# Optimization experiments

Measured on AMD Instinct MI355X. Metric: run time of the kernel, lower is better.

## Reference

```python
import jax, jax.numpy as jnp
import numpy as np


def setup_inputs() -> dict:
    key = jax.random.key(0)
    ks = jax.random.split(key, 5)
    B, C, T, Hh, Ww = 4, 64, 8, 32, 32
    HID = 32
    s = 0.05  # weight scale for numerically sane softmax logits
    return {
        "H": jax.random.normal(ks[0], (B, C, T, Hh, Ww), dtype=jnp.float32),
        "h": jax.random.normal(ks[1], (B, C, Hh, Ww), dtype=jnp.float32),
        "w_q": jax.random.normal(ks[2], (HID, C), dtype=jnp.float32) * s,
        "w_kv": jax.random.normal(ks[3], (HID, C), dtype=jnp.float32) * s,
        "w_o": jax.random.normal(ks[4], (C, HID), dtype=jnp.float32) * s,
    }


def reference(H, h, w_q, w_kv, w_o):
    B, C, T, Hh, Ww = H.shape
    N = Hh * Ww
    Hf = H.reshape(B, C, T, N)
    # 1x1 convs are pure channel-mixing matmuls
    H_kv = jnp.einsum('dc,bctn->bdtn', w_kv, Hf)                # [B, hid, T, N]
    h_q = jnp.einsum('dc,bchw->bdhw', w_q, h).reshape(B, -1, N)  # [B, hid, N]
    h_q = h_q.transpose(0, 2, 1)                                 # [B, N, hid]
    # per-timestep scores, vectorized over t: [B, T, N, N]
    a = jnp.einsum('bnd,bdtm->btnm', h_q, H_kv)
    # remove the diagonal of each per-timestep [N, N] block
    diag = jnp.einsum('btnn->btn', a)                            # [B, T, N]
    eye = jnp.eye(N, dtype=a.dtype)
    a = a - diag[..., :, None] * eye
    # concat over t along rows, softmax over the (T*N) row axis
    att = jax.nn.softmax(a.reshape(B, T * N, N), axis=1)         # [B, T*N, N]
    h_v = jnp.einsum('bdk,bkm->bdm', H_kv.reshape(B, -1, T * N), att)  # [B, hid, N]
    h_v = jnp.einsum('cd,bdhw->bchw', w_o, h_v.reshape(B, -1, Hh, Ww))
    return (h + h_v, att)
```

## Files before the change

### kernel.cpp

```cpp
#include <hip/hip_runtime.h>

typedef short bf16x8 __attribute__((ext_vector_type(8)));
typedef float f32x4  __attribute__((ext_vector_type(4)));
typedef unsigned short ushort_t;

#define HID 32
#define CC  64
#define TT  8
#define NN  1024
#define BB  4
#define KTOT 8192
#define NKC_P 32
#define KCHUNK_P (KTOT/NKC_P)

__device__ __forceinline__ ushort_t f2b(float x) {
    unsigned int u = __float_as_uint(x);
    return (ushort_t)((u + 0x7fffu + ((u >> 16) & 1u)) >> 16);
}
__device__ __forceinline__ float b2f(ushort_t u) {
    return __uint_as_float((unsigned int)u << 16);
}

__global__ __launch_bounds__(256) void k_pre(const float* __restrict__ H,
                                             const float* __restrict__ h,
                                             const float* __restrict__ wq,
                                             const float* __restrict__ wkv,
                                             ushort_t* __restrict__ hqHI,
                                             ushort_t* __restrict__ hqLO,
                                             ushort_t* __restrict__ hkTH0,
                                             ushort_t* __restrict__ hkTH1,
                                             ushort_t* __restrict__ hkTL0,
                                             ushort_t* __restrict__ hkTL1,
                                             ushort_t* __restrict__ hkDB) {
    int bx = blockIdx.x;
    if (bx < 256) {
        int gid = bx * 256 + threadIdx.x;
        int dg = gid >> 15;
        int rest = gid & 32767;
        int b = rest >> 13, tn = rest & 8191;
        int d0 = dg << 4;
        float acc[16];
#pragma unroll
        for (int d = 0; d < 16; d++) acc[d] = 0.f;
        const float* Hb = H + (size_t)(b * CC) * KTOT + tn;
        const float* wb = wkv + d0 * CC;
#pragma unroll 8
        for (int c = 0; c < CC; c++) {
            float v = Hb[(size_t)c * KTOT];
#pragma unroll
            for (int d = 0; d < 16; d++) acc[d] += wb[d * CC + c] * v;
        }
        ushort_t thi[16], tlo[16];
#pragma unroll
        for (int d = 0; d < 16; d++) {
            ushort_t hi = f2b(acc[d]);
            thi[d] = hi;
            tlo[d] = f2b(acc[d] - b2f(hi));
        }
        size_t po = ((size_t)b * KTOT + tn) * 16;
        bf16x8* ohi = (bf16x8*)((dg ? hkTH1 : hkTH0) + po);
        bf16x8* olo = (bf16x8*)((dg ? hkTL1 : hkTL0) + po);
#pragma unroll
        for (int v8 = 0; v8 < 2; v8++) {
            bf16x8 a, l;
#pragma unroll
            for (int j = 0; j < 8; j++) { a[j] = (short)thi[v8*8+j]; l[j] = (short)tlo[v8*8+j]; }
            ohi[v8] = a; olo[v8] = l;
        }
#pragma unroll
        for (int d = 0; d < 16; d++)
            hkDB[((size_t)(b * HID) + d0 + d) * KTOT + tn] = thi[d];
    } else {
        int gid = (bx - 256) * 256 + threadIdx.x;
        int b = gid >> 10;
        float acc[HID];
#pragma unroll
        for (int d = 0; d < HID; d++) acc[d] = 0.f;
        const float* hb = h + (size_t)(b * CC) * NN + (gid & 1023);
#pragma unroll 4
        for (int c = 0; c < CC; c++) {
            float v = hb[c * NN];
#pragma unroll
            for (int d = 0; d < HID; d++) acc[d] += wq[d * CC + c] * v;
        }
        bf16x8* ohi = (bf16x8*)(hqHI + (size_t)gid * HID);
        bf16x8* olo = (bf16x8*)(hqLO + (size_t)gid * HID);
#pragma unroll
        for (int v8 = 0; v8 < 4; v8++) {
            bf16x8 thi, tlo;
#pragma unroll
            for (int j = 0; j < 8; j++) {
                float x = acc[v8 * 8 + j];
                ushort_t hi = f2b(x);
                thi[j] = (short)hi;
                tlo[j] = (short)f2b(x - b2f(hi));
            }
            ohi[v8] = thi; olo[v8] = tlo;
        }
    }
}

__global__ __launch_bounds__(512, 8) void k_psum(const ushort_t* __restrict__ hqHI,
                                                 const ushort_t* __restrict__ hkTH0,
                                                 const ushort_t* __restrict__ hkTH1,
                                                 float* __restrict__ psum) {
    int bx = blockIdx.x;
    int b = bx >> 8, mt = (bx >> 5) & 7, kc = bx & 31;
    int wave = threadIdx.x >> 6, lane = threadIdx.x & 63;
    int g = lane >> 4, c = lane & 15;
    int m = mt * 128 + wave * 16 + c;
    int t = kc >> 2;
    int nb0 = (kc & 3) << 8;

    size_t bqo = ((size_t)b * KTOT + t * NN + m) * 16 + (g & 1) * 8;
    bf16x8 bqh = *(const bf16x8*)(((g >> 1) ? hkTH1 : hkTH0) + bqo);

    const ushort_t* qhi = hqHI + ((size_t)(b << 10)) * HID;

    float csum0 = 0.f, csum1 = 0.f;
    for (int s16 = 0; s16 < KCHUNK_P / 16; s16 += 2) {
        int nbA = nb0 + s16 * 16;
        int nbB = nbA + 16;
        bf16x8 ahA = *(const bf16x8*)(qhi + (size_t)(nbA + c) * HID + 8 * g);
        bf16x8 ahB = *(const bf16x8*)(qhi + (size_t)(nbB + c) * HID + 8 * g);
        f32x4 svA = __builtin_amdgcn_mfma_f32_16x16x32_bf16(ahA, bqh, (f32x4){0.f,0.f,0.f,0.f}, 0, 0, 0);
        f32x4 svB = __builtin_amdgcn_mfma_f32_16x16x32_bf16(ahB, bqh, (f32x4){0.f,0.f,0.f,0.f}, 0, 0, 0);
        int nrowA = nbA + 4 * g;
        int nrowB = nbB + 4 * g;
#pragma unroll
        for (int r = 0; r < 4; r++) {
            float xA = (nrowA + r == m) ? 0.f : svA[r];
            float xB = (nrowB + r == m) ? 0.f : svB[r];
            csum0 += __expf(xA);
            csum1 += __expf(xB);
        }
    }
    float csum = csum0 + csum1;
    csum += __shfl_xor(csum, 16);
    csum += __shfl_xor(csum, 32);
    if (lane < 16)
        psum[(((size_t)(b * NKC_P + kc)) << 10) + mt * 128 + wave * 16 + lane] = csum;
}

__global__ __launch_bounds__(1024) void k_main(const ushort_t* __restrict__ hqHI,
                                               const ushort_t* __restrict__ hqLO,
                                               const ushort_t* __restrict__ hkTH0,
                                               const ushort_t* __restrict__ hkTH1,
                                               const ushort_t* __restrict__ hkTL0,
                                               const ushort_t* __restrict__ hkTL1,
                                               const ushort_t* __restrict__ hkDB,
                                               const float* __restrict__ psum,
                                               const float* __restrict__ h,
                                               const float* __restrict__ wo,
                                               float* __restrict__ att,
                                               float* __restrict__ out0) {
    int bx = blockIdx.x;
    int logical = ((bx & 7) << 5) | (bx >> 3);
    int b = logical >> 6, mt = logical & 63;
    int mb = mt << 4;
    int tid = threadIdx.x;
    int wave = tid >> 6, lane = tid & 63;
    int g = lane >> 4, c = lane & 15;
    int t = wave >> 1;
    int nh = (wave & 1) << 9;

    __shared__ float hvred[16][16][32];
    __shared__ float hvL[16][33];
    __shared__ __align__(16) ushort_t PT[16][16][40];

    f32x4 gs = {0.f, 0.f, 0.f, 0.f};
#pragma unroll
    for (int j = 0; j < NKC_P; j++)
        gs += *(const f32x4*)(psum + (((size_t)(b * NKC_P + j)) << 10) + mb + 4 * g);
    f32x4 vinv;
#pragma unroll
    for (int r = 0; r < 4; r++) vinv[r] = 1.0f / gs[r];

    size_t ako = ((size_t)b * KTOT + t * NN + (mb + c)) * 16 + (g & 1) * 8;
    bf16x8 akh = *(const bf16x8*)(((g >> 1) ? hkTH1 : hkTH0) + ako);
    bf16x8 akl = *(const bf16x8*)(((g >> 1) ? hkTL1 : hkTL0) + ako);

    const ushort_t* qhi = hqHI + ((size_t)(b << 10)) * HID;
    const ushort_t* qlo = hqLO + ((size_t)(b << 10)) * HID;
    const ushort_t* vb0 = hkDB + (size_t)(b * HID + c) * KTOT;
    const ushort_t* vb1 = hkDB + (size_t)(b * HID + 16 + c) * KTOT;
    float* attb = att + (size_t)b * KTOT * NN;
    ushort_t (*pt)[40] = PT[wave];

    f32x4 acc0 = {0.f,0.f,0.f,0.f}, acc1 = {0.f,0.f,0.f,0.f};

    for (int ks = 0; ks < 16; ks++) {
        int k0 = t * NN + nh + ks * 32;
#pragma unroll
        for (int half = 0; half < 2; half++) {
            int nb = nh + ks * 32 + half * 16;
            size_t qo = (size_t)(nb + c) * HID + 8 * g;
            bf16x8 qh = *(const bf16x8*)(qhi + qo);
            bf16x8 ql = *(const bf16x8*)(qlo + qo);
            f32x4 sv = __builtin_amdgcn_mfma_f32_16x16x32_bf16(akh, ql, (f32x4){0.f,0.f,0.f,0.f}, 0, 0, 0);
            sv = __builtin_amdgcn_mfma_f32_16x16x32_bf16(akl, qh, sv, 0, 0, 0);
            sv = __builtin_amdgcn_mfma_f32_16x16x32_bf16(akh, qh, sv, 0, 0, 0);
            int n = nb + c;
            float e0 = __expf((n == mb + 4 * g + 0) ? 0.f : sv[0]) * vinv[0];
            float e1 = __expf((n == mb + 4 * g + 1) ? 0.f : sv[1]) * vinv[1];
            float e2 = __expf((n == mb + 4 * g + 2) ? 0.f : sv[2]) * vinv[2];
            float e3 = __expf((n == mb + 4 * g + 3) ? 0.f : sv[3]) * vinv[3];
            f32x4 ev; ev[0] = e0; ev[1] = e1; ev[2] = e2; ev[3] = e3;
            *(f32x4*)(attb + (size_t)(t * NN + n) * NN + mb + 4 * g) = ev;
            int kl = half * 16 + c;
            pt[4 * g + 0][kl] = f2b(e0);
            pt[4 * g + 1][kl] = f2b(e1);
            pt[4 * g + 2][kl] = f2b(e2);
            pt[4 * g + 3][kl] = f2b(e3);
        }
        bf16x8 pa = *(const bf16x8*)&pt[c][8 * g];
        bf16x8 v0 = *(const bf16x8*)(vb0 + k0 + 8 * g);
        bf16x8 v1 = *(const bf16x8*)(vb1 + k0 + 8 * g);
        acc0 = __builtin_amdgcn_mfma_f32_16x16x32_bf16(pa, v0, acc0, 0, 0, 0);
        acc1 = __builtin_amdgcn_mfma_f32_16x16x32_bf16(pa, v1, acc1, 0, 0, 0);
    }

#pragma unroll
    for (int r = 0; r < 4; r++) {
        hvred[wave][4 * g + r][c]      = acc0[r];
        hvred[wave][4 * g + r][16 + c] = acc1[r];
    }
    __syncthreads();
    if (tid < 512) {
        int m = tid >> 5, d = tid & 31;
        float s = 0.f;
#pragma unroll
        for (int w = 0; w < 16; w++) s += hvred[w][m][d];
        hvL[m][d] = s;
    }
    __syncthreads();
    {
        int cc = tid >> 4, mm = tid & 15;
        float v = h[(size_t)(b * CC + cc) * NN + mb + mm];
#pragma unroll
        for (int d = 0; d < HID; d++) v += wo[cc * HID + d] * hvL[mm][d];
        out0[(size_t)(b * CC + cc) * NN + mb + mm] = v;
    }
}

extern "C" void kernel_launch(void* const* d_in, const int* in_sizes, int n_in,
                              void* d_out, int out_size, void* d_ws, size_t ws_size,
                              hipStream_t stream) {
    const float* H   = (const float*)d_in[0];
    const float* h   = (const float*)d_in[1];
    const float* wq  = (const float*)d_in[2];
    const float* wkv = (const float*)d_in[3];
    const float* wo  = (const float*)d_in[4];

    float* out0 = (float*)d_out;
    float* att  = out0 + (size_t)BB * CC * NN;

    ushort_t* hqHI  = (ushort_t*)d_ws;
    ushort_t* hqLO  = hqHI  + 131072;
    ushort_t* hkTH0 = hqLO  + 131072;
    ushort_t* hkTH1 = hkTH0 + 524288;
    ushort_t* hkTL0 = hkTH1 + 524288;
    ushort_t* hkTL1 = hkTL0 + 524288;
    ushort_t* hkDB  = hkTL1 + 524288;
    float* psum = (float*)(hkDB + 1048576);

    k_pre <<<272,  256,  0, stream>>>(H, h, wq, wkv, hqHI, hqLO,
                                      hkTH0, hkTH1, hkTL0, hkTL1, hkDB);
    k_psum<<<1024, 512,  0, stream>>>(hqHI, hkTH0, hkTH1, psum);
    k_main<<<256,  1024, 0, stream>>>(hqHI, hqLO, hkTH0, hkTH1, hkTL0, hkTL1, hkDB,
                                      psum, h, wo, att, out0);
}
```

Baseline: 85.62 us.

## Repartition k_main blocks over 32-column tiles and key halves, add output kernel

Each k_main block now covers 32 output columns and one half of the key range (n in 0-511 or 512-1023) instead of 16 columns and the full key range. Every wave now handles one timestep and one 16-column half, so the block produces a partial h_v sum for its key half. The two partial sums are written to workspace and combined in a new k_out kernel, which also applies the w_o projection and the residual add. This changes the per-block access pattern for q and att and removes the serial epilogue from k_main, at the cost of an extra launch and a workspace round trip.

```diff
diff --git a/kernel.cpp b/kernel.cpp
--- a/kernel.cpp
+++ b/kernel.cpp
@@ -150,33 +150,33 @@
                                                const ushort_t* __restrict__ hkTL1,
                                                const ushort_t* __restrict__ hkDB,
                                                const float* __restrict__ psum,
-                                               const float* __restrict__ h,
-                                               const float* __restrict__ wo,
                                                float* __restrict__ att,
-                                               float* __restrict__ out0) {
+                                               float* __restrict__ hvp) {
     int bx = blockIdx.x;
     int logical = ((bx & 7) << 5) | (bx >> 3);
-    int b = logical >> 6, mt = logical & 63;
-    int mb = mt << 4;
+    int b = logical >> 6;
+    int r6 = logical & 63;
+    int mg = r6 >> 1, kh = r6 & 1;
+    int mb32 = mg << 5;
     int tid = threadIdx.x;
     int wave = tid >> 6, lane = tid & 63;
     int g = lane >> 4, c = lane & 15;
-    int t = wave >> 1;
-    int nh = (wave & 1) << 9;
+    int t = wave >> 1, mh = wave & 1;
+    int mbw = mb32 + (mh << 4);
+    int nh = kh << 9;
 
     __shared__ float hvred[16][16][32];
-    __shared__ float hvL[16][33];
     __shared__ __align__(16) ushort_t PT[16][16][40];
 
     f32x4 gs = {0.f, 0.f, 0.f, 0.f};
 #pragma unroll
     for (int j = 0; j < NKC_P; j++)
-        gs += *(const f32x4*)(psum + (((size_t)(b * NKC_P + j)) << 10) + mb + 4 * g);
+        gs += *(const f32x4*)(psum + (((size_t)(b * NKC_P + j)) << 10) + mbw + 4 * g);
     f32x4 vinv;
 #pragma unroll
     for (int r = 0; r < 4; r++) vinv[r] = 1.0f / gs[r];
 
-    size_t ako = ((size_t)b * KTOT + t * NN + (mb + c)) * 16 + (g & 1) * 8;
+    size_t ako = ((size_t)b * KTOT + t * NN + (mbw + c)) * 16 + (g & 1) * 8;
     bf16x8 akh = *(const bf16x8*)(((g >> 1) ? hkTH1 : hkTH0) + ako);
     bf16x8 akl = *(const bf16x8*)(((g >> 1) ? hkTL1 : hkTL0) + ako);
 
@@ -201,12 +201,12 @@
             sv = __builtin_amdgcn_mfma_f32_16x16x32_bf16(akl, qh, sv, 0, 0, 0);
             sv = __builtin_amdgcn_mfma_f32_16x16x32_bf16(akh, qh, sv, 0, 0, 0);
             int n = nb + c;
-            float e0 = __expf((n == mb + 4 * g + 0) ? 0.f : sv[0]) * vinv[0];
-            float e1 = __expf((n == mb + 4 * g + 1) ? 0.f : sv[1]) * vinv[1];
-            float e2 = __expf((n == mb + 4 * g + 2) ? 0.f : sv[2]) * vinv[2];
-            float e3 = __expf((n == mb + 4 * g + 3) ? 0.f : sv[3]) * vinv[3];
+            float e0 = __expf((n == mbw + 4 * g + 0) ? 0.f : sv[0]) * vinv[0];
+            float e1 = __expf((n == mbw + 4 * g + 1) ? 0.f : sv[1]) * vinv[1];
+            float e2 = __expf((n == mbw + 4 * g + 2) ? 0.f : sv[2]) * vinv[2];
+            float e3 = __expf((n == mbw + 4 * g + 3) ? 0.f : sv[3]) * vinv[3];
             f32x4 ev; ev[0] = e0; ev[1] = e1; ev[2] = e2; ev[3] = e3;
-            *(f32x4*)(attb + (size_t)(t * NN + n) * NN + mb + 4 * g) = ev;
+            *(f32x4*)(attb + (size_t)(t * NN + n) * NN + mbw + 4 * g) = ev;
             int kl = half * 16 + c;
             pt[4 * g + 0][kl] = f2b(e0);
             pt[4 * g + 1][kl] = f2b(e1);
@@ -226,20 +226,39 @@
         hvred[wave][4 * g + r][16 + c] = acc1[r];
     }
     __syncthreads();
-    if (tid < 512) {
-        int m = tid >> 5, d = tid & 31;
+    {
+        int m32 = tid >> 5, d = tid & 31;
+        int mhh = m32 >> 4, ml = m32 & 15;
         float s = 0.f;
 #pragma unroll
-        for (int w = 0; w < 16; w++) s += hvred[w][m][d];
-        hvL[m][d] = s;
+        for (int tt = 0; tt < 8; tt++) s += hvred[tt * 2 + mhh][ml][d];
+        hvp[(((size_t)(kh * 4 + b) << 10) + mb32 + m32) * HID + d] = s;
+    }
+}
+
+__global__ __launch_bounds__(512) void k_out(const float* __restrict__ h,
+                                             const float* __restrict__ wo,
+                                             const float* __restrict__ hvp,
+                                             float* __restrict__ out0) {
+    int bx = blockIdx.x;
+    int b = bx >> 6, mt = bx & 63;
+    int m0 = mt * 16;
+    int tid = threadIdx.x;
+    __shared__ float hvL[16][33];
+    {
+        int mm = tid >> 5, d = tid & 31;
+        size_t i0 = ((size_t)(b << 10) + m0 + mm) * HID + d;
+        hvL[mm][d] = hvp[i0] + hvp[((size_t)4 << 15) + i0];
     }
     __syncthreads();
-    {
-        int cc = tid >> 4, mm = tid & 15;
-        float v = h[(size_t)(b * CC + cc) * NN + mb + mm];
-#pragma unroll
-        for (int d = 0; d < HID; d++) v += wo[cc * HID + d] * hvL[mm][d];
-        out0[(size_t)(b * CC + cc) * NN + mb + mm] = v;
+#pragma unroll
+    for (int i0 = 0; i0 < 2; i0++) {
+        int i = i0 * 512 + tid;
+        int c = i >> 4, mm = i & 15;
+        float v = h[(size_t)(b * CC + c) * NN + m0 + mm];
+#pragma unroll
+        for (int d = 0; d < HID; d++) v += wo[c * HID + d] * hvL[mm][d];
+        out0[(size_t)(b * CC + c) * NN + m0 + mm] = v;
     }
 }
 
@@ -263,10 +282,12 @@
     ushort_t* hkTL1 = hkTL0 + 524288;
     ushort_t* hkDB  = hkTL1 + 524288;
     float* psum = (float*)(hkDB + 1048576);
+    float* hvp  = psum + 131072;
 
     k_pre <<<272,  256,  0, stream>>>(H, h, wq, wkv, hqHI, hqLO,
                                       hkTH0, hkTH1, hkTL0, hkTL1, hkDB);
     k_psum<<<1024, 512,  0, stream>>>(hqHI, hkTH0, hkTH1, psum);
     k_main<<<256,  1024, 0, stream>>>(hqHI, hqLO, hkTH0, hkTH1, hkTL0, hkTL1, hkDB,
-                                      psum, h, wo, att, out0);
-}
+                                      psum, att, hvp);
+    k_out <<<256,  512,  0, stream>>>(h, wo, hvp, out0);
+}
```

Result: no change. 86.67 us (+1.2%).

## Split main kernel into hv-accumulation blocks and separate att-writer blocks

Applied to the files above, without the earlier changes.

Replaces the single main kernel with a combined launch. The first 256 blocks compute the hv accumulation at single-pass bf16 precision (only the hi parts of q and k), and the other 2048 blocks recompute scores at 3-pass precision and write the large att tensor. A small kernel now reduces the partial softmax sums to reciprocals once, so blocks no longer each re-reduce psum. The aim is to spread the store-bound att writes across many more blocks while the hv path does less MFMA work. In exchange, QK scores are computed twice, and the lower-precision P used for hv may change accuracy.

```diff
diff --git a/kernel.cpp b/kernel.cpp
--- a/kernel.cpp
+++ b/kernel.cpp
@@ -142,104 +142,149 @@
         psum[(((size_t)(b * NKC_P + kc)) << 10) + mt * 128 + wave * 16 + lane] = csum;
 }
 
-__global__ __launch_bounds__(1024) void k_main(const ushort_t* __restrict__ hqHI,
-                                               const ushort_t* __restrict__ hqLO,
-                                               const ushort_t* __restrict__ hkTH0,
-                                               const ushort_t* __restrict__ hkTH1,
-                                               const ushort_t* __restrict__ hkTL0,
-                                               const ushort_t* __restrict__ hkTL1,
-                                               const ushort_t* __restrict__ hkDB,
-                                               const float* __restrict__ psum,
-                                               const float* __restrict__ h,
-                                               const float* __restrict__ wo,
-                                               float* __restrict__ att,
-                                               float* __restrict__ out0) {
+__global__ __launch_bounds__(256) void k_inv(const float* __restrict__ psum,
+                                             float* __restrict__ inv) {
+    int gid = blockIdx.x * 256 + threadIdx.x;
+    int b = gid >> 10, m = gid & 1023;
+    float s = 0.f;
+#pragma unroll
+    for (int kc = 0; kc < NKC_P; kc++)
+        s += psum[(((size_t)(b * NKC_P + kc)) << 10) + m];
+    inv[gid] = 1.0f / s;
+}
+
+__global__ __launch_bounds__(512) void k_mega(const ushort_t* __restrict__ hqHI,
+                                              const ushort_t* __restrict__ hqLO,
+                                              const ushort_t* __restrict__ hkTH0,
+                                              const ushort_t* __restrict__ hkTH1,
+                                              const ushort_t* __restrict__ hkTL0,
+                                              const ushort_t* __restrict__ hkTL1,
+                                              const ushort_t* __restrict__ hkDB,
+                                              const float* __restrict__ inv,
+                                              const float* __restrict__ h,
+                                              const float* __restrict__ wo,
+                                              float* __restrict__ att,
+                                              float* __restrict__ out0) {
     int bx = blockIdx.x;
-    int logical = ((bx & 7) << 5) | (bx >> 3);
-    int b = logical >> 6, mt = logical & 63;
-    int mb = mt << 4;
     int tid = threadIdx.x;
     int wave = tid >> 6, lane = tid & 63;
     int g = lane >> 4, c = lane & 15;
-    int t = wave >> 1;
-    int nh = (wave & 1) << 9;
-
-    __shared__ float hvred[16][16][32];
-    __shared__ float hvL[16][33];
-    __shared__ __align__(16) ushort_t PT[16][16][40];
-
-    f32x4 gs = {0.f, 0.f, 0.f, 0.f};
-#pragma unroll
-    for (int j = 0; j < NKC_P; j++)
-        gs += *(const f32x4*)(psum + (((size_t)(b * NKC_P + j)) << 10) + mb + 4 * g);
-    f32x4 vinv;
-#pragma unroll
-    for (int r = 0; r < 4; r++) vinv[r] = 1.0f / gs[r];
-
-    size_t ako = ((size_t)b * KTOT + t * NN + (mb + c)) * 16 + (g & 1) * 8;
-    bf16x8 akh = *(const bf16x8*)(((g >> 1) ? hkTH1 : hkTH0) + ako);
-    bf16x8 akl = *(const bf16x8*)(((g >> 1) ? hkTL1 : hkTL0) + ako);
-
-    const ushort_t* qhi = hqHI + ((size_t)(b << 10)) * HID;
-    const ushort_t* qlo = hqLO + ((size_t)(b << 10)) * HID;
-    const ushort_t* vb0 = hkDB + (size_t)(b * HID + c) * KTOT;
-    const ushort_t* vb1 = hkDB + (size_t)(b * HID + 16 + c) * KTOT;
-    float* attb = att + (size_t)b * KTOT * NN;
-    ushort_t (*pt)[40] = PT[wave];
-
-    f32x4 acc0 = {0.f,0.f,0.f,0.f}, acc1 = {0.f,0.f,0.f,0.f};
-
-    for (int ks = 0; ks < 16; ks++) {
-        int k0 = t * NN + nh + ks * 32;
-#pragma unroll
-        for (int half = 0; half < 2; half++) {
-            int nb = nh + ks * 32 + half * 16;
+
+    if (bx < 256) {
+        int logical = ((bx & 7) << 5) | (bx >> 3);
+        int b = logical >> 6, mt = logical & 63;
+        int mb = mt << 4;
+        int t = wave;
+
+        __shared__ float hvred[8][16][32];
+        __shared__ float hvL[16][33];
+        __shared__ __align__(16) ushort_t PT[8][16][40];
+
+        f32x4 vinv = *(const f32x4*)(inv + (b << 10) + mb + 4 * g);
+
+        size_t ako = ((size_t)b * KTOT + t * NN + (mb + c)) * 16 + (g & 1) * 8;
+        bf16x8 akh = *(const bf16x8*)(((g >> 1) ? hkTH1 : hkTH0) + ako);
+
+        const ushort_t* qhi = hqHI + ((size_t)(b << 10)) * HID;
+        const ushort_t* vb0 = hkDB + (size_t)(b * HID + c) * KTOT;
+        const ushort_t* vb1 = hkDB + (size_t)(b * HID + 16 + c) * KTOT;
+        ushort_t (*pt)[40] = PT[wave];
+
+        f32x4 acc0 = {0.f,0.f,0.f,0.f}, acc1 = {0.f,0.f,0.f,0.f};
+        for (int ks = 0; ks < 32; ks++) {
+            int k0 = t * NN + ks * 32;
+#pragma unroll
+            for (int half = 0; half < 2; half++) {
+                int nb = ks * 32 + half * 16;
+                size_t qo = (size_t)(nb + c) * HID + 8 * g;
+                bf16x8 qh = *(const bf16x8*)(qhi + qo);
+                f32x4 sv = __builtin_amdgcn_mfma_f32_16x16x32_bf16(akh, qh, (f32x4){0.f,0.f,0.f,0.f}, 0, 0, 0);
+                int n = nb + c;
+                float e0 = __expf((n == mb + 4 * g + 0) ? 0.f : sv[0]) * vinv[0];
+                float e1 = __expf((n == mb + 4 * g + 1) ? 0.f : sv[1]) * vinv[1];
+                float e2 = __expf((n == mb + 4 * g + 2) ? 0.f : sv[2]) * vinv[2];
+                float e3 = __expf((n == mb + 4 * g + 3) ? 0.f : sv[3]) * vinv[3];
+                int kl = half * 16 + c;
+                pt[4 * g + 0][kl] = f2b(e0);
+                pt[4 * g + 1][kl] = f2b(e1);
+                pt[4 * g + 2][kl] = f2b(e2);
+                pt[4 * g + 3][kl] = f2b(e3);
+            }
+            bf16x8 pa = *(const bf16x8*)&pt[c][8 * g];
+            bf16x8 v0 = *(const bf16x8*)(vb0 + k0 + 8 * g);
+            bf16x8 v1 = *(const bf16x8*)(vb1 + k0 + 8 * g);
+            acc0 = __builtin_amdgcn_mfma_f32_16x16x32_bf16(pa, v0, acc0, 0, 0, 0);
+            acc1 = __builtin_amdgcn_mfma_f32_16x16x32_bf16(pa, v1, acc1, 0, 0, 0);
+        }
+#pragma unroll
+        for (int r = 0; r < 4; r++) {
+            hvred[wave][4 * g + r][c]      = acc0[r];
+            hvred[wave][4 * g + r][16 + c] = acc1[r];
+        }
+        __syncthreads();
+        {
+            int m = tid >> 5, d = tid & 31;
+            float s = 0.f;
+#pragma unroll
+            for (int w = 0; w < 8; w++) s += hvred[w][m][d];
+            hvL[m][d] = s;
+        }
+        __syncthreads();
+#pragma unroll
+        for (int i0 = 0; i0 < 2; i0++) {
+            int i = i0 * 512 + tid;
+            int cc = i >> 4, mm = i & 15;
+            float v = h[(size_t)(b * CC + cc) * NN + mb + mm];
+#pragma unroll
+            for (int d = 0; d < HID; d++) v += wo[cc * HID + d] * hvL[mm][d];
+            out0[(size_t)(b * CC + cc) * NN + mb + mm] = v;
+        }
+    } else {
+        int axid = bx - 256;
+        int logical = ((axid & 7) << 8) | (axid >> 3);
+        int b = logical >> 9;
+        int r9 = logical & 511;
+        int t = r9 >> 6;
+        int r6 = r9 & 63;
+        int ng = r6 >> 1, ch = r6 & 1;
+        int mf = (ch << 9) + (wave << 6);
+
+        bf16x8 akh[4], akl[4];
+        f32x4 vinv[4];
+#pragma unroll
+        for (int f = 0; f < 4; f++) {
+            size_t ako = ((size_t)b * KTOT + t * NN + (mf + 16 * f + c)) * 16 + (g & 1) * 8;
+            akh[f] = *(const bf16x8*)(((g >> 1) ? hkTH1 : hkTH0) + ako);
+            akl[f] = *(const bf16x8*)(((g >> 1) ? hkTL1 : hkTL0) + ako);
+            vinv[f] = *(const f32x4*)(inv + (b << 10) + mf + 16 * f + 4 * g);
+        }
+
+        const ushort_t* qhi = hqHI + ((size_t)(b << 10)) * HID;
+        const ushort_t* qlo = hqLO + ((size_t)(b << 10)) * HID;
+        float* attb = att + (size_t)b * KTOT * NN;
+
+#pragma unroll
+        for (int ks = 0; ks < 2; ks++) {
+            int nb = ng * 32 + ks * 16;
             size_t qo = (size_t)(nb + c) * HID + 8 * g;
             bf16x8 qh = *(const bf16x8*)(qhi + qo);
             bf16x8 ql = *(const bf16x8*)(qlo + qo);
-            f32x4 sv = __builtin_amdgcn_mfma_f32_16x16x32_bf16(akh, ql, (f32x4){0.f,0.f,0.f,0.f}, 0, 0, 0);
-            sv = __builtin_amdgcn_mfma_f32_16x16x32_bf16(akl, qh, sv, 0, 0, 0);
-            sv = __builtin_amdgcn_mfma_f32_16x16x32_bf16(akh, qh, sv, 0, 0, 0);
             int n = nb + c;
-            float e0 = __expf((n == mb + 4 * g + 0) ? 0.f : sv[0]) * vinv[0];
-            float e1 = __expf((n == mb + 4 * g + 1) ? 0.f : sv[1]) * vinv[1];
-            float e2 = __expf((n == mb + 4 * g + 2) ? 0.f : sv[2]) * vinv[2];
-            float e3 = __expf((n == mb + 4 * g + 3) ? 0.f : sv[3]) * vinv[3];
-            f32x4 ev; ev[0] = e0; ev[1] = e1; ev[2] = e2; ev[3] = e3;
-            *(f32x4*)(attb + (size_t)(t * NN + n) * NN + mb + 4 * g) = ev;
-            int kl = half * 16 + c;
-            pt[4 * g + 0][kl] = f2b(e0);
-            pt[4 * g + 1][kl] = f2b(e1);
-            pt[4 * g + 2][kl] = f2b(e2);
-            pt[4 * g + 3][kl] = f2b(e3);
-        }
-        bf16x8 pa = *(const bf16x8*)&pt[c][8 * g];
-        bf16x8 v0 = *(const bf16x8*)(vb0 + k0 + 8 * g);
-        bf16x8 v1 = *(const bf16x8*)(vb1 + k0 + 8 * g);
-        acc0 = __builtin_amdgcn_mfma_f32_16x16x32_bf16(pa, v0, acc0, 0, 0, 0);
-        acc1 = __builtin_amdgcn_mfma_f32_16x16x32_bf16(pa, v1, acc1, 0, 0, 0);
-    }
-
-#pragma unroll
-    for (int r = 0; r < 4; r++) {
-        hvred[wave][4 * g + r][c]      = acc0[r];
-        hvred[wave][4 * g + r][16 + c] = acc1[r];
-    }
-    __syncthreads();
-    if (tid < 512) {
-        int m = tid >> 5, d = tid & 31;
-        float s = 0.f;
-#pragma unroll
-        for (int w = 0; w < 16; w++) s += hvred[w][m][d];
-        hvL[m][d] = s;
-    }
-    __syncthreads();
-    {
-        int cc = tid >> 4, mm = tid & 15;
-        float v = h[(size_t)(b * CC + cc) * NN + mb + mm];
-#pragma unroll
-        for (int d = 0; d < HID; d++) v += wo[cc * HID + d] * hvL[mm][d];
-        out0[(size_t)(b * CC + cc) * NN + mb + mm] = v;
+            float* rowp = attb + (size_t)(t * NN + n) * NN;
+#pragma unroll
+            for (int f = 0; f < 4; f++) {
+                f32x4 sv = __builtin_amdgcn_mfma_f32_16x16x32_bf16(akh[f], ql, (f32x4){0.f,0.f,0.f,0.f}, 0, 0, 0);
+                sv = __builtin_amdgcn_mfma_f32_16x16x32_bf16(akl[f], qh, sv, 0, 0, 0);
+                sv = __builtin_amdgcn_mfma_f32_16x16x32_bf16(akh[f], qh, sv, 0, 0, 0);
+                int mrow = mf + 16 * f + 4 * g;
+                f32x4 ev;
+                ev[0] = __expf((n == mrow + 0) ? 0.f : sv[0]) * vinv[f][0];
+                ev[1] = __expf((n == mrow + 1) ? 0.f : sv[1]) * vinv[f][1];
+                ev[2] = __expf((n == mrow + 2) ? 0.f : sv[2]) * vinv[f][2];
+                ev[3] = __expf((n == mrow + 3) ? 0.f : sv[3]) * vinv[f][3];
+                *(f32x4*)(rowp + mrow) = ev;
+            }
+        }
     }
 }
 
@@ -263,10 +308,12 @@
     ushort_t* hkTL1 = hkTL0 + 524288;
     ushort_t* hkDB  = hkTL1 + 524288;
     float* psum = (float*)(hkDB + 1048576);
-
-    k_pre <<<272,  256,  0, stream>>>(H, h, wq, wkv, hqHI, hqLO,
-                                      hkTH0, hkTH1, hkTL0, hkTL1, hkDB);
-    k_psum<<<1024, 512,  0, stream>>>(hqHI, hkTH0, hkTH1, psum);
-    k_main<<<256,  1024, 0, stream>>>(hqHI, hqLO, hkTH0, hkTH1, hkTL0, hkTL1, hkDB,
-                                      psum, h, wo, att, out0);
-}
+    float* inv  = psum + 131072;
+
+    k_pre <<<272,  256, 0, stream>>>(H, h, wq, wkv, hqHI, hqLO,
+                                     hkTH0, hkTH1, hkTL0, hkTL1, hkDB);
+    k_psum<<<1024, 512, 0, stream>>>(hqHI, hkTH0, hkTH1, psum);
+    k_inv <<<16,   256, 0, stream>>>(psum, inv);
+    k_mega<<<2304, 512, 0, stream>>>(hqHI, hqLO, hkTH0, hkTH1, hkTL0, hkTL1, hkDB,
+                                     inv, h, wo, att, out0);
+}
```

Result: slower. 88.72 us (+3.6%).
